# Kernel tuning notes

Hardware: AMD Instinct MI355X
Metric: run time of the kernel (lower is better)

## Reference

```python
import jax, jax.numpy as jnp
import numpy as np

NUM_HEADS = 16

def _w8a8_linear(x_q, x_scale, w_q, w_scale, bias):
    # W8A8 GEMM with dynamic per-token input scale and per-output-channel weight scale
    # x_q: [N, Din] int8 values, w_q: [Dout, Din] int8 values
    acc = jnp.matmul(x_q.astype(jnp.float32), w_q.astype(jnp.float32).T)  # [N, Dout]
    return acc * (x_scale[:, None] * w_scale[None, :]) + bias[None, :]


def setup_inputs() -> dict:
    key = jax.random.key(0)
    ks = jax.random.split(key, 16)
    B, S, D = 2, 2048, 1024
    N = B * S
    def int8(k, shape):
        return jax.random.randint(k, shape, -127, 128, dtype=jnp.int32)
    inp = {
        "x_q": int8(ks[0], (N, D)),
        "x_scale": jax.random.uniform(ks[1], (N,), jnp.float32, 0.005, 0.02),
        "wq": int8(ks[2], (D, D)),
        "wq_scale": jax.random.uniform(ks[3], (D,), jnp.float32, 0.005, 0.02),
        "bq": jax.random.normal(ks[4], (D,), jnp.float32) * 0.02,
        "wk": int8(ks[5], (D, D)),
        "wk_scale": jax.random.uniform(ks[6], (D,), jnp.float32, 0.005, 0.02),
        "bk": jax.random.normal(ks[7], (D,), jnp.float32) * 0.02,
        "wv": int8(ks[8], (D, D)),
        "wv_scale": jax.random.uniform(ks[9], (D,), jnp.float32, 0.005, 0.02),
        "bv": jax.random.normal(ks[10], (D,), jnp.float32) * 0.02,
        "wo": int8(ks[11], (D, D)),
        "wo_scale": jax.random.uniform(ks[12], (D,), jnp.float32, 0.005, 0.02),
        "bo": jax.random.normal(ks[13], (D,), jnp.float32) * 0.02,
        "bsz": B,
        "qlen": S,
    }
    return inp


def reference(x_q, x_scale, wq, wq_scale, bq, wk, wk_scale, bk,
              wv, wv_scale, bv, wo, wo_scale, bo, bsz, qlen):
    D = wq.shape[0]
    hd = D // NUM_HEADS
    # quantized QKV projections (dequant fused into GEMM epilogue)
    q = _w8a8_linear(x_q, x_scale, wq, wq_scale, bq).reshape(bsz, qlen, NUM_HEADS, hd)
    k = _w8a8_linear(x_q, x_scale, wk, wk_scale, bk).reshape(bsz, qlen, NUM_HEADS, hd)
    v = _w8a8_linear(x_q, x_scale, wv, wv_scale, bv).reshape(bsz, qlen, NUM_HEADS, hd)
    # flash_attn_func(softmax_scale=None, causal=False) => scale = 1/sqrt(head_dim)
    scale = 1.0 / jnp.sqrt(jnp.float32(hd))
    scores = jnp.einsum('bqhd,bkhd->bhqk', q, k) * scale
    probs = jax.nn.softmax(scores, axis=-1)
    attn = jnp.einsum('bhqk,bkhd->bqhd', probs, v).reshape(bsz * qlen, D)
    # invoke_quant: dynamic per-token symmetric int8 quantization of attn output
    o_scale = jnp.max(jnp.abs(attn), axis=-1) / 127.0  # [N]
    o_q = jnp.clip(jnp.round(attn / o_scale[:, None]), -127.0, 127.0)
    # quantized out projection
    out = _w8a8_linear(o_q, o_scale, wo, wo_scale, bo)  # [N, D]
    return out
```

## Files before the change

kernel.cpp:

```cpp
#include <hip/hip_runtime.h>

#define D_MODEL 1024
#define NTOK    4096
#define SEQ     2048
#define NH      16
#define HD      64

typedef __bf16 bh8  __attribute__((ext_vector_type(8)));
typedef __bf16 bf4  __attribute__((ext_vector_type(4)));
typedef float  f32x4 __attribute__((ext_vector_type(4)));
typedef int    i32x4 __attribute__((ext_vector_type(4)));

__device__ __forceinline__ unsigned short f2bf(float f) {
  unsigned int u = __float_as_uint(f);
  u += 0x7fffu + ((u >> 16) & 1u);
  return (unsigned short)(u >> 16);
}
__device__ __forceinline__ float exp2a(float x) {
  float r; asm("v_exp_f32 %0, %1" : "=v"(r) : "v"(x)); return r;
}
__device__ __forceinline__ void gl16(const void* g, void* l) {
  __builtin_amdgcn_global_load_lds((const __attribute__((address_space(1))) unsigned int*)g,
                                   (__attribute__((address_space(3))) unsigned int*)l, 16, 0, 0);
}

__device__ __forceinline__ void pack_row(const int* src, unsigned* dst, int m, int t) {
  int4 w = *(const int4*)(src + (size_t)m * 1024 + t * 4);
  unsigned p01 = __builtin_amdgcn_perm((unsigned)w.y, (unsigned)w.x, 0x00000400u);
  unsigned p23 = __builtin_amdgcn_perm((unsigned)w.w, (unsigned)w.z, 0x00000400u);
  unsigned r   = __builtin_amdgcn_perm(p23, p01, 0x05040100u);
  int kg = t >> 4, c = (t >> 2) & 3, b4 = t & 3, sw = (m >> 1) & 3;
  dst[(size_t)m * 256 + kg * 16 + ((c ^ sw) << 2) + b4] = r;
}
__launch_bounds__(256)
__global__ void pack_k(const int* __restrict__ x,
                       const int* __restrict__ s0, const int* __restrict__ s1,
                       const int* __restrict__ s2, const int* __restrict__ s3,
                       unsigned* __restrict__ dx,
                       unsigned* __restrict__ d0, unsigned* __restrict__ d1,
                       unsigned* __restrict__ d2, unsigned* __restrict__ d3) {
  int bid = blockIdx.x;
  if (bid < 4096) { pack_row(x, dx, bid, threadIdx.x); return; }
  bid -= 4096;
  int wsel = bid >> 10, m = bid & 1023;
  const int* src = wsel == 0 ? s0 : wsel == 1 ? s1 : wsel == 2 ? s2 : s3;
  unsigned*  dst = wsel == 0 ? d0 : wsel == 1 ? d1 : wsel == 2 ? d2 : d3;
  pack_row(src, dst, m, threadIdx.x);
}

__launch_bounds__(256, 2)
__global__ void gemmQKV_k(const signed char* __restrict__ xp,
                          const signed char* __restrict__ wqp,
                          const signed char* __restrict__ wkp,
                          const signed char* __restrict__ wvp,
                          const float* __restrict__ xs,
                          const float* __restrict__ wqs, const float* __restrict__ bq,
                          const float* __restrict__ wks, const float* __restrict__ bk,
                          const float* __restrict__ wvs, const float* __restrict__ bv,
                          float SC,
                          signed char* __restrict__ qp8h, signed char* __restrict__ qp8l,
                          signed char* __restrict__ kp8h, signed char* __restrict__ kp8l,
                          float* __restrict__ sq, float* __restrict__ sk,
                          unsigned short* __restrict__ vtw)
{
  __shared__ __align__(16) signed char As[2][8192];
  __shared__ __align__(16) signed char Bs[2][4096];
  const int id = blockIdx.x, z = id >> 9, rb = id & 511;
  const int t = threadIdx.x, wid = t >> 6, lane = t & 63, g = lane >> 4, li = lane & 15;
  const signed char *Ap, *Bp;
  int m0, n0;
  if (z == 2) { Ap = wvp; Bp = xp; m0 = (rb >> 6) * 128; n0 = (rb & 63) * 64; }
  else        { Ap = xp; Bp = z ? wkp : wqp; m0 = (rb >> 4) * 128; n0 = (rb & 15) * 64; }

  i32x4 acc[2][4];
#pragma unroll
  for (int i = 0; i < 2; ++i)
#pragma unroll
    for (int j = 0; j < 4; ++j) acc[i][j] = (i32x4){0, 0, 0, 0};

#pragma unroll
  for (int i = 0; i < 2; ++i) {
    int unit = (wid * 2 + i) * 64 + lane, r = unit >> 2, c = unit & 3;
    gl16(Ap + (size_t)(m0 + r) * 1024 + c * 16, (char*)As[0] + (wid * 2 + i) * 1024);
  }
  { int unit = wid * 64 + lane, r = unit >> 2, c = unit & 3;
    gl16(Bp + (size_t)(n0 + r) * 1024 + c * 16, (char*)Bs[0] + wid * 1024); }
  __syncthreads();
  int p = 0;
#pragma unroll 1
  for (int ks = 0; ks < 16; ++ks) {
    if (ks < 15) {
      const int k0 = (ks + 1) * 64;
#pragma unroll
      for (int i = 0; i < 2; ++i) {
        int unit = (wid * 2 + i) * 64 + lane, r = unit >> 2, c = unit & 3;
        gl16(Ap + (size_t)(m0 + r) * 1024 + k0 + c * 16, (char*)As[p ^ 1] + (wid * 2 + i) * 1024);
      }
      { int unit = wid * 64 + lane, r = unit >> 2, c = unit & 3;
        gl16(Bp + (size_t)(n0 + r) * 1024 + k0 + c * 16, (char*)Bs[p ^ 1] + wid * 1024); }
    }
    i32x4 af[2], bfr[4];
#pragma unroll
    for (int mt = 0; mt < 2; ++mt) {
      int row = wid * 32 + mt * 16 + li;
      af[mt] = *(const i32x4*)(As[p] + row * 64 + ((g ^ ((row >> 1) & 3)) << 4));
    }
#pragma unroll
    for (int nt = 0; nt < 4; ++nt) {
      int row = nt * 16 + li;
      bfr[nt] = *(const i32x4*)(Bs[p] + row * 64 + ((g ^ ((row >> 1) & 3)) << 4));
    }
    __builtin_amdgcn_s_setprio(1);
#pragma unroll
    for (int mt = 0; mt < 2; ++mt)
#pragma unroll
      for (int nt = 0; nt < 4; ++nt)
        acc[mt][nt] = __builtin_amdgcn_mfma_i32_16x16x64_i8(af[mt], bfr[nt], acc[mt][nt], 0, 0, 0);
    __builtin_amdgcn_s_setprio(0);
    __syncthreads();
    p ^= 1;
  }

  if (z == 2) {
#pragma unroll
    for (int mt = 0; mt < 2; ++mt)
#pragma unroll
      for (int nt = 0; nt < 4; ++nt) {
        const int nn = n0 + nt * 16 + li;
#pragma unroll
        for (int r = 0; r < 4; ++r) {
          const int m = m0 + wid * 32 + mt * 16 + g * 4 + r;
          float f = (float)acc[mt][nt][r] * (wvs[m] * xs[nn]) + bv[m];
          int hh = m >> 6, d = m & 63, bb = nn >> 11, s = nn & 2047;
          int ss = (s & ~63) | (((((s >> 3) & 7) ^ (d & 7)) << 3) | (s & 7));
          vtw[(((size_t)(bb * NH + hh)) * HD + d) * SEQ + ss] = f2bf(f);
        }
      }
  } else {
    const float* wsc = z ? wks : wqs;
    const float* wbi = z ? bk : bq;
    signed char* dh = z ? kp8h : qp8h;
    signed char* dl = z ? kp8l : qp8l;
    float*       sc = z ? sk : sq;
    const int head = (n0 >> 6) & 15;
    float ws4[4], wb4[4];
#pragma unroll
    for (int nt = 0; nt < 4; ++nt) { ws4[nt] = wsc[n0 + nt * 16 + li]; wb4[nt] = wbi[n0 + nt * 16 + li]; }
#pragma unroll
    for (int mt = 0; mt < 2; ++mt) {
      float4 xs4 = *(const float4*)(xs + m0 + wid * 32 + mt * 16 + g * 4);
      float xa[4] = {xs4.x, xs4.y, xs4.z, xs4.w};
#pragma unroll
      for (int r = 0; r < 4; ++r) {
        const int m = m0 + wid * 32 + mt * 16 + g * 4 + r;
        float f[4];
#pragma unroll
        for (int nt = 0; nt < 4; ++nt) {
          f[nt] = fmaf((float)acc[mt][nt][r], xa[r] * ws4[nt], wb4[nt]);
          if (z == 0) f[nt] *= SC;
        }
        float mx = fmaxf(fmaxf(fabsf(f[0]), fabsf(f[1])), fmaxf(fabsf(f[2]), fabsf(f[3])));
        mx = fmaxf(mx, __shfl_xor(mx, 1));
        mx = fmaxf(mx, __shfl_xor(mx, 2));
        mx = fmaxf(mx, __shfl_xor(mx, 4));
        mx = fmaxf(mx, __shfl_xor(mx, 8));
        mx = fmaxf(mx, 1e-20f);
        const float inv = 32512.0f / mx;
        const int bb = m >> 11, sR = m & 2047;
        const size_t rowo = ((size_t)(bb * NH + head) * SEQ + sR) * 64;
#pragma unroll
        for (int nt = 0; nt < 4; ++nt) {
          int qi = (int)rintf(f[nt] * inv);
          int qh = (qi + 128) >> 8;
          int ql = qi - (qh << 8);
          int d = nt * 16 + li;
          int dd = z ? ((((d >> 4) ^ (m & 3)) << 4) | (d & 15)) : d;
          dh[rowo + dd] = (signed char)qh;
          dl[rowo + dd] = (signed char)ql;
        }
        if (li == 0) sc[(size_t)(bb * NH + head) * SEQ + sR] = mx * (1.0f / 32512.0f);
      }
    }
  }
}

__launch_bounds__(256, 2)
__global__ void gemmO_k(const signed char* __restrict__ Ap, const signed char* __restrict__ Bp,
                        const float* __restrict__ sA, const float* __restrict__ sB,
                        const float* __restrict__ bias, float* __restrict__ outF)
{
  __shared__ __align__(16) signed char As[2][8192];
  __shared__ __align__(16) signed char Bs[2][4096];
  const int id = blockIdx.x;
  const int m0 = (id >> 4) * 128, n0 = (id & 15) * 64;
  const int t = threadIdx.x, wid = t >> 6, lane = t & 63, g = lane >> 4, li = lane & 15;

  i32x4 acc[2][4];
#pragma unroll
  for (int i = 0; i < 2; ++i)
#pragma unroll
    for (int j = 0; j < 4; ++j) acc[i][j] = (i32x4){0, 0, 0, 0};

#pragma unroll
  for (int i = 0; i < 2; ++i) {
    int unit = (wid * 2 + i) * 64 + lane, r = unit >> 2, c = unit & 3;
    gl16(Ap + (size_t)(m0 + r) * 1024 + c * 16, (char*)As[0] + (wid * 2 + i) * 1024);
  }
  { int unit = wid * 64 + lane, r = unit >> 2, c = unit & 3;
    gl16(Bp + (size_t)(n0 + r) * 1024 + c * 16, (char*)Bs[0] + wid * 1024); }
  __syncthreads();
  int p = 0;
#pragma unroll 1
  for (int ks = 0; ks < 16; ++ks) {
    if (ks < 15) {
      const int k0 = (ks + 1) * 64;
#pragma unroll
      for (int i = 0; i < 2; ++i) {
        int unit = (wid * 2 + i) * 64 + lane, r = unit >> 2, c = unit & 3;
        gl16(Ap + (size_t)(m0 + r) * 1024 + k0 + c * 16, (char*)As[p ^ 1] + (wid * 2 + i) * 1024);
      }
      { int unit = wid * 64 + lane, r = unit >> 2, c = unit & 3;
        gl16(Bp + (size_t)(n0 + r) * 1024 + k0 + c * 16, (char*)Bs[p ^ 1] + wid * 1024); }
    }
    i32x4 af[2], bfr[4];
#pragma unroll
    for (int mt = 0; mt < 2; ++mt) {
      int row = wid * 32 + mt * 16 + li;
      af[mt] = *(const i32x4*)(As[p] + row * 64 + ((g ^ ((row >> 1) & 3)) << 4));
    }
#pragma unroll
    for (int nt = 0; nt < 4; ++nt) {
      int row = nt * 16 + li;
      bfr[nt] = *(const i32x4*)(Bs[p] + row * 64 + ((g ^ ((row >> 1) & 3)) << 4));
    }
    __builtin_amdgcn_s_setprio(1);
#pragma unroll
    for (int mt = 0; mt < 2; ++mt)
#pragma unroll
      for (int nt = 0; nt < 4; ++nt)
        acc[mt][nt] = __builtin_amdgcn_mfma_i32_16x16x64_i8(af[mt], bfr[nt], acc[mt][nt], 0, 0, 0);
    __builtin_amdgcn_s_setprio(0);
    __syncthreads();
    p ^= 1;
  }

#pragma unroll
  for (int mt = 0; mt < 2; ++mt)
#pragma unroll
    for (int nt = 0; nt < 4; ++nt) {
      const int nn = n0 + nt * 16 + li;
#pragma unroll
      for (int r = 0; r < 4; ++r) {
        const int m = m0 + wid * 32 + mt * 16 + g * 4 + r;
        outF[(size_t)m * 1024 + nn] = (float)acc[mt][nt][r] * (sA[m] * sB[nn]) + bias[nn];
      }
    }
}

__launch_bounds__(256, 2)
__global__ void attn_k(const signed char* __restrict__ qp8h, const signed char* __restrict__ qp8l,
                       const signed char* __restrict__ kp8h, const signed char* __restrict__ kp8l,
                       const float* __restrict__ sq, const float* __restrict__ sk,
                       const unsigned short* __restrict__ vt, float* __restrict__ attn)
{
  __shared__ __align__(16) signed char kbh[2][4096], kbl[2][4096];
  __shared__ __align__(16) unsigned short vts[2][4096];
  __shared__ __align__(16) unsigned short ps[4][2][1024];
  const int t = threadIdx.x;
  const int w = t >> 6, lane = t & 63, g = lane >> 4, li = lane & 15;
  const int q0 = blockIdx.x * 128, h = blockIdx.y, b = blockIdx.z;
  const int bh = b * NH + h;
  const int qA = q0 + w * 32 + li, qB = qA + 16;

  i32x4 qh8[2], ql8[2];
  qh8[0] = *(const i32x4*)(qp8h + ((size_t)bh * SEQ + qA) * 64 + g * 16);
  ql8[0] = *(const i32x4*)(qp8l + ((size_t)bh * SEQ + qA) * 64 + g * 16);
  qh8[1] = *(const i32x4*)(qp8h + ((size_t)bh * SEQ + qB) * 64 + g * 16);
  ql8[1] = *(const i32x4*)(qp8l + ((size_t)bh * SEQ + qB) * 64 + g * 16);
  const float sqv[2] = { sq[(size_t)bh * SEQ + qA], sq[(size_t)bh * SEQ + qB] };
  const signed char* kbg = kp8h + (size_t)bh * SEQ * 64;
  const signed char* klg = kp8l + (size_t)bh * SEQ * 64;
  const float* skg = sk + (size_t)bh * SEQ;
  const unsigned short* vb = vt + (size_t)bh * HD * SEQ;

  float m_run[2] = {-INFINITY, -INFINITY}, l_run[2] = {0.0f, 0.0f};
  f32x4 ot[2][4];
#pragma unroll
  for (int s = 0; s < 2; ++s)
#pragma unroll
    for (int i = 0; i < 4; ++i) ot[s][i] = (f32x4)0.0f;

  {
    int u = w * 64 + lane, r = u >> 2, c = u & 3;
    gl16(kbg + r * 64 + c * 16, (char*)kbh[0] + w * 1024);
    gl16(klg + r * 64 + c * 16, (char*)kbl[0] + w * 1024);
#pragma unroll
    for (int i = 0; i < 2; ++i) {
      int u2 = (w * 2 + i) * 64 + lane, rv = u2 >> 3, cv = u2 & 7;
      gl16(vb + (size_t)rv * SEQ + cv * 8, (char*)vts[0] + (w * 2 + i) * 1024);
    }
  }

#pragma unroll 1
  for (int it = 0; it < 32; ++it) {
    const int kk0 = it * 64, cur = it & 1;
    __syncthreads();
    i32x4 kh[4], kl[4];
#pragma unroll
    for (int kt2 = 0; kt2 < 4; ++kt2) {
      int row = kt2 * 16 + li, co = (g ^ (row & 3)) << 4;
      kh[kt2] = *(const i32x4*)(kbh[cur] + row * 64 + co);
      kl[kt2] = *(const i32x4*)(kbl[cur] + row * 64 + co);
    }
    if (it < 31) {
      int u = w * 64 + lane, r = u >> 2, c = u & 3;
      gl16(kbg + (size_t)(kk0 + 64 + r) * 64 + c * 16, (char*)kbh[cur ^ 1] + w * 1024);
      gl16(klg + (size_t)(kk0 + 64 + r) * 64 + c * 16, (char*)kbl[cur ^ 1] + w * 1024);
#pragma unroll
      for (int i = 0; i < 2; ++i) {
        int u2 = (w * 2 + i) * 64 + lane, rv = u2 >> 3, cv = u2 & 7;
        gl16(vb + (size_t)rv * SEQ + kk0 + 64 + cv * 8, (char*)vts[cur ^ 1] + (w * 2 + i) * 1024);
      }
    }
    f32x4 sa[2][4];
#pragma unroll
    for (int kt2 = 0; kt2 < 4; ++kt2) {
      float4 sk4 = *(const float4*)(skg + kk0 + kt2 * 16 + g * 4);
      float ska[4] = {sk4.x, sk4.y, sk4.z, sk4.w};
#pragma unroll
      for (int s = 0; s < 2; ++s) {
        i32x4 z4 = (i32x4){0, 0, 0, 0};
        __builtin_amdgcn_s_setprio(1);
        i32x4 hh = __builtin_amdgcn_mfma_i32_16x16x64_i8(kh[kt2], qh8[s], z4, 0, 0, 0);
        i32x4 mm = __builtin_amdgcn_mfma_i32_16x16x64_i8(kl[kt2], qh8[s], z4, 0, 0, 0);
        mm = __builtin_amdgcn_mfma_i32_16x16x64_i8(kh[kt2], ql8[s], mm, 0, 0, 0);
        i32x4 ll = __builtin_amdgcn_mfma_i32_16x16x64_i8(kl[kt2], ql8[s], z4, 0, 0, 0);
        __builtin_amdgcn_s_setprio(0);
#pragma unroll
        for (int r = 0; r < 4; ++r) {
          int A = (hh[r] << 8) + mm[r];
          sa[s][kt2][r] = fmaf((float)A, 256.0f, (float)ll[r]) * (sqv[s] * ska[r]);
        }
      }
    }
#pragma unroll
    for (int s = 0; s < 2; ++s) {
      float sm = -INFINITY;
#pragma unroll
      for (int kt2 = 0; kt2 < 4; ++kt2)
#pragma unroll
        for (int r = 0; r < 4; ++r) sm = fmaxf(sm, sa[s][kt2][r]);
      sm = fmaxf(sm, __shfl_xor(sm, 16));
      sm = fmaxf(sm, __shfl_xor(sm, 32));
      if (__any(sm > m_run[s] + 11.0f)) {
        float mn = fmaxf(m_run[s], sm);
        float alpha = exp2a(m_run[s] - mn);
        l_run[s] *= alpha;
#pragma unroll
        for (int i = 0; i < 4; ++i) ot[s][i] *= alpha;
        m_run[s] = mn;
      }
      float ts = 0.0f;
#pragma unroll
      for (int kt2 = 0; kt2 < 4; ++kt2)
#pragma unroll
        for (int r = 0; r < 4; ++r) {
          float e = exp2a(sa[s][kt2][r] - m_run[s]);
          sa[s][kt2][r] = e; ts += e;
        }
      ts += __shfl_xor(ts, 16);
      ts += __shfl_xor(ts, 32);
      l_run[s] += ts;
#pragma unroll
      for (int kt2 = 0; kt2 < 4; ++kt2) {
        bf4 pk = { (__bf16)sa[s][kt2][0], (__bf16)sa[s][kt2][1],
                   (__bf16)sa[s][kt2][2], (__bf16)sa[s][kt2][3] };
        int lchunk = (kt2 << 1) | (g >> 1);
        *(bf4*)((char*)ps[w][s] + li * 128 + ((lchunk ^ (li & 7)) << 4) + ((g & 1) << 3)) = pk;
      }
    }
    asm volatile("s_waitcnt lgkmcnt(0)" ::: "memory");
    __builtin_amdgcn_sched_barrier(0);
    bh8 pf[2][2];
#pragma unroll
    for (int s = 0; s < 2; ++s)
#pragma unroll
      for (int kc2 = 0; kc2 < 2; ++kc2)
        pf[s][kc2] = *(const bh8*)((const char*)ps[w][s] + li * 128 + ((((kc2 << 2) | g) ^ (li & 7)) << 4));
#pragma unroll
    for (int kc2 = 0; kc2 < 2; ++kc2) {
      __builtin_amdgcn_s_setprio(1);
#pragma unroll
      for (int dt = 0; dt < 4; ++dt) {
        int rowd = dt * 16 + li;
        bh8 vf = *(const bh8*)((const char*)vts[cur] + rowd * 128 + ((((kc2 << 2) | g) ^ (rowd & 7)) << 4));
        ot[0][dt] = __builtin_amdgcn_mfma_f32_16x16x32_bf16(vf, pf[0][kc2], ot[0][dt], 0, 0, 0);
        ot[1][dt] = __builtin_amdgcn_mfma_f32_16x16x32_bf16(vf, pf[1][kc2], ot[1][dt], 0, 0, 0);
      }
      __builtin_amdgcn_s_setprio(0);
    }
  }

#pragma unroll
  for (int s = 0; s < 2; ++s) {
    const float inv = 1.0f / l_run[s];
    const int n = b * SEQ + (s ? qB : qA);
#pragma unroll
    for (int dt = 0; dt < 4; ++dt) {
      float4 o4;
      o4.x = ot[s][dt][0] * inv; o4.y = ot[s][dt][1] * inv;
      o4.z = ot[s][dt][2] * inv; o4.w = ot[s][dt][3] * inv;
      *(float4*)(attn + (size_t)n * D_MODEL + h * HD + dt * 16 + g * 4) = o4;
    }
  }
}

__launch_bounds__(256)
__global__ void quant_k(const float* __restrict__ attn, unsigned* __restrict__ oqp,
                        float* __restrict__ osc)
{
  const int row = blockIdx.x, t = threadIdx.x;
  float4 v = *(const float4*)(attn + (size_t)row * D_MODEL + t * 4);
  float mx = fmaxf(fmaxf(fabsf(v.x), fabsf(v.y)), fmaxf(fabsf(v.z), fabsf(v.w)));
#pragma unroll
  for (int off = 1; off < 64; off <<= 1) mx = fmaxf(mx, __shfl_xor(mx, off));
  __shared__ float red[4];
  if ((t & 63) == 0) red[t >> 6] = mx;
  __syncthreads();
  mx = fmaxf(fmaxf(red[0], red[1]), fmaxf(red[2], red[3]));
  const float s = mx / 127.0f;
  if (t == 0) osc[row] = s;
  int q0 = (int)fminf(fmaxf(rintf(v.x / s), -127.f), 127.f);
  int q1 = (int)fminf(fmaxf(rintf(v.y / s), -127.f), 127.f);
  int q2 = (int)fminf(fmaxf(rintf(v.z / s), -127.f), 127.f);
  int q3 = (int)fminf(fmaxf(rintf(v.w / s), -127.f), 127.f);
  unsigned pk = ((unsigned)q0 & 255u) | (((unsigned)q1 & 255u) << 8) |
                (((unsigned)q2 & 255u) << 16) | (((unsigned)q3 & 255u) << 24);
  int kg = t >> 4, c = (t >> 2) & 3, b4 = t & 3, sw = (row >> 1) & 3;
  oqp[(size_t)row * 256 + kg * 16 + ((c ^ sw) << 2) + b4] = pk;
}

extern "C" void kernel_launch(void* const* d_in, const int* in_sizes, int n_in,
                              void* d_out, int out_size, void* d_ws, size_t ws_size,
                              hipStream_t stream)
{
  const int*   x   = (const int*)d_in[0];
  const float* xs  = (const float*)d_in[1];
  const int*   wq  = (const int*)d_in[2];
  const float* wqs = (const float*)d_in[3];
  const float* bq  = (const float*)d_in[4];
  const int*   wk  = (const int*)d_in[5];
  const float* wks = (const float*)d_in[6];
  const float* bk  = (const float*)d_in[7];
  const int*   wv  = (const int*)d_in[8];
  const float* wvs = (const float*)d_in[9];
  const float* bv  = (const float*)d_in[10];
  const int*   wo  = (const int*)d_in[11];
  const float* wos = (const float*)d_in[12];
  const float* bo  = (const float*)d_in[13];
  float* out = (float*)d_out;

  char* ws = (char*)d_ws;
  const size_t MB = 1024 * 1024;
  unsigned* xp  = (unsigned*)(ws);
  unsigned* wqp = (unsigned*)(ws + 4 * MB);
  unsigned* wkp = (unsigned*)(ws + 5 * MB);
  unsigned* wvp = (unsigned*)(ws + 6 * MB);
  unsigned* wop = (unsigned*)(ws + 7 * MB);
  signed char* qp8h = (signed char*)(ws + 8 * MB);
  signed char* qp8l = (signed char*)(ws + 12 * MB);
  signed char* kp8h = (signed char*)(ws + 16 * MB);
  signed char* kp8l = (signed char*)(ws + 20 * MB);
  float*       sqs  = (float*)(ws + 24 * MB);
  float*       sks  = (float*)(ws + 24 * MB + 256 * 1024);
  unsigned short* vtw = (unsigned short*)(ws + 25 * MB);
  float*          att = (float*)(ws + 33 * MB);
  unsigned*       oqp = (unsigned*)(ws);
  float*          osc = (float*)(ws + 4 * MB);

  const float SC = 0.125f * 1.44269504088896340736f;
  dim3 blk(256);
  pack_k<<<dim3(8192), blk, 0, stream>>>(x, wq, wk, wv, wo, xp, wqp, wkp, wvp, wop);
  gemmQKV_k<<<dim3(1536), blk, 0, stream>>>((const signed char*)xp, (const signed char*)wqp,
                                            (const signed char*)wkp, (const signed char*)wvp,
                                            xs, wqs, bq, wks, bk, wvs, bv, SC,
                                            qp8h, qp8l, kp8h, kp8l, sqs, sks, vtw);
  attn_k<<<dim3(16, NH, 2), blk, 0, stream>>>(qp8h, qp8l, kp8h, kp8l, sqs, sks, vtw, att);
  quant_k<<<dim3(4096), blk, 0, stream>>>(att, oqp, osc);
  gemmO_k<<<dim3(512), blk, 0, stream>>>((const signed char*)oqp, (const signed char*)wop,
                                         osc, wos, bo, out);
}
```

Before: 244.4 us.

## Enlarge QKV GEMM tiles to 128x128 with 2x2 wave layout

The fused QKV GEMM block tile grows from 128x64 to 128x128, with waves arranged 2x2 and each wave computing a 64x64 sub-tile (4x4 MFMA fragments). The grid halves to 768 blocks. This raises operand reuse per LDS load and cuts global traffic per output. The K-buffer swizzle is changed to use (row>>1)&3 in both the QKV epilogue and attention reads, keeping producer and consumer layouts matched. The cost is more accumulator registers per thread and fewer blocks to spread across CUs.

```diff
diff --git a/kernel.cpp b/kernel.cpp
--- a/kernel.cpp
+++ b/kernel.cpp
@@ -64,27 +64,28 @@
                           unsigned short* __restrict__ vtw)
 {
   __shared__ __align__(16) signed char As[2][8192];
-  __shared__ __align__(16) signed char Bs[2][4096];
-  const int id = blockIdx.x, z = id >> 9, rb = id & 511;
+  __shared__ __align__(16) signed char Bs[2][8192];
+  const int id = blockIdx.x, z = id >> 8, rb = id & 255;
   const int t = threadIdx.x, wid = t >> 6, lane = t & 63, g = lane >> 4, li = lane & 15;
+  const int wm = wid >> 1, wn = wid & 1;
   const signed char *Ap, *Bp;
   int m0, n0;
-  if (z == 2) { Ap = wvp; Bp = xp; m0 = (rb >> 6) * 128; n0 = (rb & 63) * 64; }
-  else        { Ap = xp; Bp = z ? wkp : wqp; m0 = (rb >> 4) * 128; n0 = (rb & 15) * 64; }
-
-  i32x4 acc[2][4];
-#pragma unroll
-  for (int i = 0; i < 2; ++i)
+  if (z == 2) { Ap = wvp; Bp = xp; m0 = (rb & 7) * 128; n0 = (rb >> 3) * 128; }
+  else        { Ap = xp; Bp = z ? wkp : wqp; m0 = (rb >> 3) * 128; n0 = (rb & 7) * 128; }
+
+  i32x4 acc[4][4];
+#pragma unroll
+  for (int i = 0; i < 4; ++i)
 #pragma unroll
     for (int j = 0; j < 4; ++j) acc[i][j] = (i32x4){0, 0, 0, 0};
 
+  const int unitBase = wid * 2;
 #pragma unroll
   for (int i = 0; i < 2; ++i) {
-    int unit = (wid * 2 + i) * 64 + lane, r = unit >> 2, c = unit & 3;
-    gl16(Ap + (size_t)(m0 + r) * 1024 + c * 16, (char*)As[0] + (wid * 2 + i) * 1024);
-  }
-  { int unit = wid * 64 + lane, r = unit >> 2, c = unit & 3;
-    gl16(Bp + (size_t)(n0 + r) * 1024 + c * 16, (char*)Bs[0] + wid * 1024); }
+    int unit = (unitBase + i) * 64 + lane, r = unit >> 2, c = unit & 3;
+    gl16(Ap + (size_t)(m0 + r) * 1024 + c * 16, (char*)As[0] + (unitBase + i) * 1024);
+    gl16(Bp + (size_t)(n0 + r) * 1024 + c * 16, (char*)Bs[0] + (unitBase + i) * 1024);
+  }
   __syncthreads();
   int p = 0;
 #pragma unroll 1
@@ -93,26 +94,25 @@
       const int k0 = (ks + 1) * 64;
 #pragma unroll
       for (int i = 0; i < 2; ++i) {
-        int unit = (wid * 2 + i) * 64 + lane, r = unit >> 2, c = unit & 3;
-        gl16(Ap + (size_t)(m0 + r) * 1024 + k0 + c * 16, (char*)As[p ^ 1] + (wid * 2 + i) * 1024);
-      }
-      { int unit = wid * 64 + lane, r = unit >> 2, c = unit & 3;
-        gl16(Bp + (size_t)(n0 + r) * 1024 + k0 + c * 16, (char*)Bs[p ^ 1] + wid * 1024); }
-    }
-    i32x4 af[2], bfr[4];
-#pragma unroll
-    for (int mt = 0; mt < 2; ++mt) {
-      int row = wid * 32 + mt * 16 + li;
+        int unit = (unitBase + i) * 64 + lane, r = unit >> 2, c = unit & 3;
+        gl16(Ap + (size_t)(m0 + r) * 1024 + k0 + c * 16, (char*)As[p ^ 1] + (unitBase + i) * 1024);
+        gl16(Bp + (size_t)(n0 + r) * 1024 + k0 + c * 16, (char*)Bs[p ^ 1] + (unitBase + i) * 1024);
+      }
+    }
+    i32x4 af[4], bfr[4];
+#pragma unroll
+    for (int mt = 0; mt < 4; ++mt) {
+      int row = wm * 64 + mt * 16 + li;
       af[mt] = *(const i32x4*)(As[p] + row * 64 + ((g ^ ((row >> 1) & 3)) << 4));
     }
 #pragma unroll
     for (int nt = 0; nt < 4; ++nt) {
-      int row = nt * 16 + li;
+      int row = wn * 64 + nt * 16 + li;
       bfr[nt] = *(const i32x4*)(Bs[p] + row * 64 + ((g ^ ((row >> 1) & 3)) << 4));
     }
     __builtin_amdgcn_s_setprio(1);
 #pragma unroll
-    for (int mt = 0; mt < 2; ++mt)
+    for (int mt = 0; mt < 4; ++mt)
 #pragma unroll
       for (int nt = 0; nt < 4; ++nt)
         acc[mt][nt] = __builtin_amdgcn_mfma_i32_16x16x64_i8(af[mt], bfr[nt], acc[mt][nt], 0, 0, 0);
@@ -123,13 +123,13 @@
 
   if (z == 2) {
 #pragma unroll
-    for (int mt = 0; mt < 2; ++mt)
+    for (int mt = 0; mt < 4; ++mt)
 #pragma unroll
       for (int nt = 0; nt < 4; ++nt) {
-        const int nn = n0 + nt * 16 + li;
+        const int nn = n0 + wn * 64 + nt * 16 + li;
 #pragma unroll
         for (int r = 0; r < 4; ++r) {
-          const int m = m0 + wid * 32 + mt * 16 + g * 4 + r;
+          const int m = m0 + wm * 64 + mt * 16 + g * 4 + r;
           float f = (float)acc[mt][nt][r] * (wvs[m] * xs[nn]) + bv[m];
           int hh = m >> 6, d = m & 63, bb = nn >> 11, s = nn & 2047;
           int ss = (s & ~63) | (((((s >> 3) & 7) ^ (d & 7)) << 3) | (s & 7));
@@ -142,17 +142,20 @@
     signed char* dh = z ? kp8h : qp8h;
     signed char* dl = z ? kp8l : qp8l;
     float*       sc = z ? sk : sq;
-    const int head = (n0 >> 6) & 15;
+    const int head = ((n0 + wn * 64) >> 6) & 15;
     float ws4[4], wb4[4];
 #pragma unroll
-    for (int nt = 0; nt < 4; ++nt) { ws4[nt] = wsc[n0 + nt * 16 + li]; wb4[nt] = wbi[n0 + nt * 16 + li]; }
-#pragma unroll
-    for (int mt = 0; mt < 2; ++mt) {
-      float4 xs4 = *(const float4*)(xs + m0 + wid * 32 + mt * 16 + g * 4);
+    for (int nt = 0; nt < 4; ++nt) {
+      ws4[nt] = wsc[n0 + wn * 64 + nt * 16 + li];
+      wb4[nt] = wbi[n0 + wn * 64 + nt * 16 + li];
+    }
+#pragma unroll
+    for (int mt = 0; mt < 4; ++mt) {
+      float4 xs4 = *(const float4*)(xs + m0 + wm * 64 + mt * 16 + g * 4);
       float xa[4] = {xs4.x, xs4.y, xs4.z, xs4.w};
 #pragma unroll
       for (int r = 0; r < 4; ++r) {
-        const int m = m0 + wid * 32 + mt * 16 + g * 4 + r;
+        const int m = m0 + wm * 64 + mt * 16 + g * 4 + r;
         float f[4];
 #pragma unroll
         for (int nt = 0; nt < 4; ++nt) {
@@ -174,7 +177,7 @@
           int qh = (qi + 128) >> 8;
           int ql = qi - (qh << 8);
           int d = nt * 16 + li;
-          int dd = z ? ((((d >> 4) ^ (m & 3)) << 4) | (d & 15)) : d;
+          int dd = z ? ((((d >> 4) ^ ((m >> 1) & 3)) << 4) | (d & 15)) : d;
           dh[rowo + dd] = (signed char)qh;
           dl[rowo + dd] = (signed char)ql;
         }
@@ -289,6 +292,7 @@
   for (int s = 0; s < 2; ++s)
 #pragma unroll
     for (int i = 0; i < 4; ++i) ot[s][i] = (f32x4)0.0f;
+  const i32x4 ZERO = (i32x4){0, 0, 0, 0};
 
   {
     int u = w * 64 + lane, r = u >> 2, c = u & 3;
@@ -308,7 +312,7 @@
     i32x4 kh[4], kl[4];
 #pragma unroll
     for (int kt2 = 0; kt2 < 4; ++kt2) {
-      int row = kt2 * 16 + li, co = (g ^ (row & 3)) << 4;
+      int row = kt2 * 16 + li, co = (g ^ ((row >> 1) & 3)) << 4;
       kh[kt2] = *(const i32x4*)(kbh[cur] + row * 64 + co);
       kl[kt2] = *(const i32x4*)(kbl[cur] + row * 64 + co);
     }
@@ -329,12 +333,11 @@
       float ska[4] = {sk4.x, sk4.y, sk4.z, sk4.w};
 #pragma unroll
       for (int s = 0; s < 2; ++s) {
-        i32x4 z4 = (i32x4){0, 0, 0, 0};
         __builtin_amdgcn_s_setprio(1);
-        i32x4 hh = __builtin_amdgcn_mfma_i32_16x16x64_i8(kh[kt2], qh8[s], z4, 0, 0, 0);
-        i32x4 mm = __builtin_amdgcn_mfma_i32_16x16x64_i8(kl[kt2], qh8[s], z4, 0, 0, 0);
+        i32x4 hh = __builtin_amdgcn_mfma_i32_16x16x64_i8(kh[kt2], qh8[s], ZERO, 0, 0, 0);
+        i32x4 mm = __builtin_amdgcn_mfma_i32_16x16x64_i8(kl[kt2], qh8[s], ZERO, 0, 0, 0);
         mm = __builtin_amdgcn_mfma_i32_16x16x64_i8(kh[kt2], ql8[s], mm, 0, 0, 0);
-        i32x4 ll = __builtin_amdgcn_mfma_i32_16x16x64_i8(kl[kt2], ql8[s], z4, 0, 0, 0);
+        i32x4 ll = __builtin_amdgcn_mfma_i32_16x16x64_i8(kl[kt2], ql8[s], ZERO, 0, 0, 0);
         __builtin_amdgcn_s_setprio(0);
 #pragma unroll
         for (int r = 0; r < 4; ++r) {
@@ -481,10 +484,10 @@
   const float SC = 0.125f * 1.44269504088896340736f;
   dim3 blk(256);
   pack_k<<<dim3(8192), blk, 0, stream>>>(x, wq, wk, wv, wo, xp, wqp, wkp, wvp, wop);
-  gemmQKV_k<<<dim3(1536), blk, 0, stream>>>((const signed char*)xp, (const signed char*)wqp,
-                                            (const signed char*)wkp, (const signed char*)wvp,
-                                            xs, wqs, bq, wks, bk, wvs, bv, SC,
-                                            qp8h, qp8l, kp8h, kp8l, sqs, sks, vtw);
+  gemmQKV_k<<<dim3(768), blk, 0, stream>>>((const signed char*)xp, (const signed char*)wqp,
+                                           (const signed char*)wkp, (const signed char*)wvp,
+                                           xs, wqs, bq, wks, bk, wvs, bv, SC,
+                                           qp8h, qp8l, kp8h, kp8l, sqs, sks, vtw);
   attn_k<<<dim3(16, NH, 2), blk, 0, stream>>>(qp8h, qp8l, kp8h, kp8l, sqs, sks, vtw, att);
   quant_k<<<dim3(4096), blk, 0, stream>>>(att, oqp, osc);
   gemmO_k<<<dim3(512), blk, 0, stream>>>((const signed char*)oqp, (const signed char*)wop,
```

Result: faster. 239.4 us (-2.0%).
